# Optimization experiments

Measured on AMD Instinct MI355X. Metric: run time of the kernel, lower is better.

Reference implementation:

```python
import jax, jax.numpy as jnp
import numpy as np

B, N_ANG, LX, LY, LZ = 2, 120, 128, 128, 128


def _rotate_z(vol, phi):
    """Rotate vol [B,Lx,Ly,Lz] by phi radians (counterclockwise) in the (x,y)
    plane about the grid center, bilinear interpolation, zero padding.
    Mirrors pytomography's rotate_detector_z (bilinear grid-sample rotate)."""
    Lx, Ly = vol.shape[1], vol.shape[2]
    dt = vol.dtype
    cx = (Lx - 1) / 2.0
    cy = (Ly - 1) / 2.0
    xs = jnp.arange(Lx, dtype=dt) - cx
    ys = jnp.arange(Ly, dtype=dt) - cy
    X, Y = jnp.meshgrid(xs, ys, indexing="ij")  # [Lx,Ly]
    c, s = jnp.cos(phi), jnp.sin(phi)
    # inverse rotation maps each output pixel to its source location
    sx = c * X + s * Y + cx
    sy = -s * X + c * Y + cy
    x0 = jnp.floor(sx)
    y0 = jnp.floor(sy)
    wx = (sx - x0)[None, :, :, None]
    wy = (sy - y0)[None, :, :, None]
    x0i = x0.astype(jnp.int32)
    y0i = y0.astype(jnp.int32)

    def gather(xi, yi):
        valid = (xi >= 0) & (xi < Lx) & (yi >= 0) & (yi < Ly)
        xic = jnp.clip(xi, 0, Lx - 1)
        yic = jnp.clip(yi, 0, Ly - 1)
        v = vol[:, xic, yic, :]  # [B,Lx,Ly,Lz]
        return v * valid.astype(dt)[None, :, :, None]

    v00 = gather(x0i, y0i)
    v01 = gather(x0i, y0i + 1)
    v10 = gather(x0i + 1, y0i)
    v11 = gather(x0i + 1, y0i + 1)
    return (v00 * (1 - wx) * (1 - wy) + v01 * (1 - wx) * wy
            + v10 * wx * (1 - wy) + v11 * wx * wy)


def setup_inputs() -> dict:
    key = jax.random.key(0)
    image = jax.random.uniform(key, (B, N_ANG, LY, LZ), dtype=jnp.float32)
    angles = jnp.linspace(0.0, 360.0, N_ANG, endpoint=False).astype(jnp.float32)
    return {"image": image, "angles": angles}


def reference(image, angles, delta=1e-11):
    # image: [B, N_angles, Lr, Lz]; angles in degrees.
    Bn, Na, Lr, Lz = image.shape
    Lx = Ly = Lr
    dt = image.dtype
    phis = -jnp.deg2rad(angles).astype(dt)  # negative=True -> back-rotation

    def step(carry, inp):
        obj_acc, norm_acc = carry
        proj, phi = inp  # proj: [B, Lr, Lz]
        # image[:, i].unsqueeze(1) * ones([B, Lx, Ly, Lz]): broadcast along x
        obj_i = jnp.broadcast_to(proj[:, None, :, :], (Bn, Lx, Ly, Lz))
        norm_i = jnp.ones((Bn, Lx, Ly, Lz), dt)
        obj_acc = obj_acc + _rotate_z(obj_i, phi)
        norm_acc = norm_acc + _rotate_z(norm_i, phi)
        return (obj_acc, norm_acc), None

    init = (jnp.zeros((Bn, Lx, Ly, Lz), dt), jnp.zeros((Bn, Lx, Ly, Lz), dt))
    (obj, norm), _ = jax.lax.scan(step, init, (jnp.swapaxes(image, 0, 1), phis))
    return obj / (norm + jnp.asarray(delta, dt))
```

## Files before the change

### kernel.cpp

```cpp
#include <hip/hip_runtime.h>

namespace {

constexpr int L     = 128;
constexpr int NANG  = 120;
constexpr int NPTS  = 16;
constexpr size_t H16_BYTES = (size_t)2 * NANG * L * L * 2;

typedef __fp16 f16x2 __attribute__((ext_vector_type(2)));
typedef __fp16 f16x4 __attribute__((ext_vector_type(4)));
typedef float  f32x4 __attribute__((ext_vector_type(4)));

__global__ __launch_bounds__(256) void cvt16_kernel(const float* __restrict__ in,
                                                    unsigned* __restrict__ out) {
    const int i = ((int)blockIdx.x * 256 + (int)threadIdx.x) * 4;
    const float4 v = *reinterpret_cast<const float4*>(in + i);
    f16x2 a = __builtin_amdgcn_cvt_pkrtz(v.x, v.y);
    f16x2 b = __builtin_amdgcn_cvt_pkrtz(v.z, v.w);
    uint2 st;
    st.x = *reinterpret_cast<unsigned*>(&a);
    st.y = *reinterpret_cast<unsigned*>(&b);
    *reinterpret_cast<uint2*>(out + i / 2) = st;
}

template <bool F16>
__global__ __launch_bounds__(512, 8) void bp_kernel(
    const void* __restrict__ imgv,
    const float* __restrict__ angles,
    float* __restrict__ out)
{
    constexpr unsigned SLICE = F16 ? 32768u : 65536u;
    constexpr unsigned ROWB  = F16 ? 256u  : 512u;
    constexpr int      RSH   = F16 ? 8 : 9;

    __shared__ alignas(16) unsigned long long aftab[NANG * 2 * NPTS];
    __shared__ float2   acs[NANG];
    __shared__ unsigned arloB[NANG];
    __shared__ alignas(16) float nrmtab[NPTS];

    const int tid = threadIdx.x;
    const int bid = (int)blockIdx.x;
    const int n   = ((bid & 7) << 7) | (bid >> 3);
    int xt = 0, yt = 0;
#pragma unroll
    for (int i = 0; i < 5; ++i) {
        xt |= ((n >> (2 * i)) & 1) << i;
        yt |= ((n >> (2 * i + 1)) & 1) << i;
    }
    const int xb = xt * 4, yb = yt * 4;
    const float cx = (L - 1) * 0.5f;

    if (tid < NANG) {
        const float phi = -angles[tid] * 0.017453292519943295f;
        float s, c;
        sincosf(phi, &s, &c);
        const float X0 = (float)xb - cx,  X1 = (float)(xb + 3) - cx;
        const float Y0 = (float)yb - cx,  Y1 = (float)(yb + 3) - cx;
        const float a00 = -s * X0 + c * Y0 + cx;
        const float a01 = -s * X0 + c * Y1 + cx;
        const float a10 = -s * X1 + c * Y0 + cx;
        const float a11 = -s * X1 + c * Y1 + cx;
        const float symin = fminf(fminf(a00, a01), fminf(a10, a11));
        acs[tid]   = make_float2(c, s);
        arloB[tid] = (unsigned)min(max((int)floorf(symin) - 1, 0), 120) << RSH;
    }
    if (tid < NPTS) nrmtab[tid] = 0.f;
    __syncthreads();

    float wsum = 0.f;
#pragma unroll
    for (int k = 0; k < 4; ++k) {
        const int e = tid + k * 512;
        if (e < NANG * NPTS) {
            const int p = e & 15;
            const int a = e >> 4;
            const float2 cs = acs[a];
            const int rlo = (int)(arloB[a] >> RSH);
            const float X = (float)(xb + (p >> 2)) - cx;
            const float Y = (float)(yb + (p & 3)) - cx;
            const float sx =  cs.x * X + cs.y * Y + cx;
            const float sy = -cs.y * X + cs.x * Y + cx;
            const float x0f = floorf(sx), y0f = floorf(sy);
            const float wx = sx - x0f,    wy = sy - y0f;
            const int x0 = (int)x0f, y0 = (int)y0f;
            const float mx0 = (x0 >= 0  && x0 <  L)     ? 1.f : 0.f;
            const float mx1 = (x0 >= -1 && x0 <= L - 2) ? 1.f : 0.f;
            const float my0 = (y0 >= 0  && y0 <  L)     ? 1.f : 0.f;
            const float my1 = (y0 >= -1 && y0 <= L - 2) ? 1.f : 0.f;
            const float A   = (1.f - wx) * mx0 + wx * mx1;
            float w0f = (1.f - wy) * my0 * A;
            float w1f = wy * my1 * A;
            const int y0c = min(max(y0, 0), L - 1);
            const int y1c = min(max(y0 + 1, 0), L - 1);
            const int s0  = min(max(y0c - rlo, 0), 7);
            const int s1  = min(max(y1c - rlo, 0), 7);
            if (s0 == s1) { w0f += w1f; w1f = 0.f; }
            f16x2 wh = __builtin_amdgcn_cvt_pkrtz(w0f, w1f);
            const unsigned wbits = *reinterpret_cast<unsigned*>(&wh);
            const unsigned t  = (unsigned)s0 & 3u;
            const int      q0 = s0 >> 2;
            const unsigned long long W = (unsigned long long)wbits << (t * 16u);
            const unsigned long long spill =
                (t == 3u) ? (unsigned long long)(wbits >> 16) : 0ull;
            aftab[a * 32 + p]      = (q0 == 0) ? W : 0ull;
            aftab[a * 32 + 16 + p] = (q0 == 1) ? W : spill;
            wsum += w0f + w1f;
        }
    }
    atomicAdd(&nrmtab[tid & 15], wsum);
    __syncthreads();

    const int wave  = tid >> 6;
    const int lane  = tid & 63;
    const int quad  = lane >> 4;
    const int lhalf = lane & 15;
    const int sel   = quad >> 1;
    const int lq    = quad & 1;
    const int b     = wave & 1;
    const int zq2   = wave >> 1;
    const char* __restrict__ imgc = (const char*)imgv;

    const unsigned bbase_s = __builtin_amdgcn_readfirstlane((unsigned)(b * NANG) * SLICE);
    const unsigned voffc = (unsigned)sel * SLICE
                         + (unsigned)(lq * 4) * ROWB
                         + (unsigned)(zq2 * 32 + 2 * lhalf) * (F16 ? 2u : 4u);

    f32x4 acc[2] = {};

    auto issue = [&](unsigned* r, float2* rfp, unsigned long long& afs, int pr) {
        afs = aftab[pr * 64 + lane];
        const unsigned rlB = arloB[2 * pr + sel];
        const char* pa = imgc + (bbase_s + (unsigned)(2 * pr) * SLICE);
        const unsigned voff = voffc + rlB;
        if constexpr (F16) {
#pragma unroll
            for (int j = 0; j < 4; ++j)
                r[j] = *(const unsigned*)(pa + (voff + (unsigned)j * ROWB));
        } else {
#pragma unroll
            for (int j = 0; j < 4; ++j)
                rfp[j] = *(const float2*)(pa + (voff + (unsigned)j * ROWB));
        }
    };
    auto compute = [&](const unsigned* r, const float2* rfp, unsigned long long afu) {
        union { unsigned long long u; f16x4 v; } c; c.u = afu;
        f16x4 bf0, bf1;
        if constexpr (F16) {
            union { unsigned u[2]; f16x4 v; } b0, b1;
            b0.u[0] = __builtin_amdgcn_perm(r[1], r[0], 0x05040100u);
            b0.u[1] = __builtin_amdgcn_perm(r[3], r[2], 0x05040100u);
            b1.u[0] = __builtin_amdgcn_perm(r[1], r[0], 0x07060302u);
            b1.u[1] = __builtin_amdgcn_perm(r[3], r[2], 0x07060302u);
            bf0 = b0.v; bf1 = b1.v;
        } else {
            const f16x2 h0a = __builtin_amdgcn_cvt_pkrtz(rfp[0].x, rfp[1].x);
            const f16x2 h0b = __builtin_amdgcn_cvt_pkrtz(rfp[2].x, rfp[3].x);
            const f16x2 h1a = __builtin_amdgcn_cvt_pkrtz(rfp[0].y, rfp[1].y);
            const f16x2 h1b = __builtin_amdgcn_cvt_pkrtz(rfp[2].y, rfp[3].y);
            bf0 = f16x4{h0a.x, h0a.y, h0b.x, h0b.y};
            bf1 = f16x4{h1a.x, h1a.y, h1b.x, h1b.y};
        }
        acc[0] = __builtin_amdgcn_mfma_f32_16x16x16f16(c.v, bf0, acc[0], 0, 0, 0);
        acc[1] = __builtin_amdgcn_mfma_f32_16x16x16f16(c.v, bf1, acc[1], 0, 0, 0);
    };

    unsigned ru0[4], ru1[4], ru2[4], ru3[4];
    float2   rf0[4], rf1[4], rf2[4], rf3[4];
    unsigned long long af0, af1, af2, af3;

    issue(ru0, rf0, af0, 0);
    issue(ru1, rf1, af1, 1);
    issue(ru2, rf2, af2, 2);

    for (int p = 0; p < 60; p += 4) {
        if (p + 3 < 60) issue(ru3, rf3, af3, p + 3);
        compute(ru0, rf0, af0);
        if (p + 4 < 60) issue(ru0, rf0, af0, p + 4);
        compute(ru1, rf1, af1);
        if (p + 5 < 60) issue(ru1, rf1, af1, p + 5);
        compute(ru2, rf2, af2);
        if (p + 6 < 60) issue(ru2, rf2, af2, p + 6);
        compute(ru3, rf3, af3);
    }

    const float4 nrm4 = *(const float4*)&nrmtab[quad * 4];
    const float iv[4] = { 1.f / (nrm4.x + 1e-11f), 1.f / (nrm4.y + 1e-11f),
                          1.f / (nrm4.z + 1e-11f), 1.f / (nrm4.w + 1e-11f) };
    const int zb = zq2 * 32 + 2 * lhalf;
#pragma unroll
    for (int r = 0; r < 4; ++r) {
        const int pnt = quad * 4 + r;
        const int x = xb + (pnt >> 2);
        const int y = yb + (pnt & 3);
        const float2 o = make_float2(acc[0][r] * iv[r], acc[1][r] * iv[r]);
        *reinterpret_cast<float2*>(&out[(((size_t)(b * L + x)) * L + y) * L + zb]) = o;
    }
}

}

extern "C" void kernel_launch(void* const* d_in, const int* in_sizes, int n_in,
                              void* d_out, int out_size, void* d_ws, size_t ws_size,
                              hipStream_t stream) {
    const float* image  = (const float*)d_in[0];
    const float* angles = (const float*)d_in[1];
    float* out = (float*)d_out;
    (void)in_sizes; (void)n_in; (void)out_size;

    dim3 grid(1024);
    if (d_ws != nullptr && ws_size >= H16_BYTES) {
        cvt16_kernel<<<dim3(3840), 256, 0, stream>>>(image, (unsigned*)d_ws);
        bp_kernel<true><<<grid, 512, 0, stream>>>(d_ws, angles, out);
    } else {
        bp_kernel<false><<<grid, 512, 0, stream>>>(image, angles, out);
    }
}
```

Before: 102.0 us.

## Split angle loop across wave groups with LDS reduction and wider z loads

Each wave now covers 64 z-values with 8-byte (f16) or 16-byte (f32) loads and four MFMA accumulators instead of two, and the eight waves split into two sets that each process half the angle pairs. The partial sums from the second set are reduced through LDS, reusing the angle table buffer, before the first set normalizes and writes float4 outputs. The aim is a shorter serial dependency chain per wave and wider memory transactions. In exchange it adds more accumulator registers, two block barriers and an LDS reduction, and half the waves sit idle during the final write.

```diff
diff --git a/kernel.cpp b/kernel.cpp
--- a/kernel.cpp
+++ b/kernel.cpp
@@ -117,17 +117,20 @@
     const int sel   = quad >> 1;
     const int lq    = quad & 1;
     const int b     = wave & 1;
-    const int zq2   = wave >> 1;
+    const int zh    = (wave >> 1) & 1;
+    const int aset  = wave >> 2;
     const char* __restrict__ imgc = (const char*)imgv;
 
     const unsigned bbase_s = __builtin_amdgcn_readfirstlane((unsigned)(b * NANG) * SLICE);
     const unsigned voffc = (unsigned)sel * SLICE
                          + (unsigned)(lq * 4) * ROWB
-                         + (unsigned)(zq2 * 32 + 2 * lhalf) * (F16 ? 2u : 4u);
-
-    f32x4 acc[2] = {};
-
-    auto issue = [&](unsigned* r, float2* rfp, unsigned long long& afs, int pr) {
+                         + (unsigned)(zh * 64 + 4 * lhalf) * (F16 ? 2u : 4u);
+    const int p0 = aset * 30;
+
+    f32x4 acc[4] = {};
+
+    auto issue = [&](uint2* r, float4* rfp, unsigned long long& afs, int i) {
+        const int pr = p0 + i;
         afs = aftab[pr * 64 + lane];
         const unsigned rlB = arloB[2 * pr + sel];
         const char* pa = imgc + (bbase_s + (unsigned)(2 * pr) * SLICE);
@@ -135,65 +138,86 @@
         if constexpr (F16) {
 #pragma unroll
             for (int j = 0; j < 4; ++j)
-                r[j] = *(const unsigned*)(pa + (voff + (unsigned)j * ROWB));
+                r[j] = *(const uint2*)(pa + (voff + (unsigned)j * ROWB));
         } else {
 #pragma unroll
             for (int j = 0; j < 4; ++j)
-                rfp[j] = *(const float2*)(pa + (voff + (unsigned)j * ROWB));
+                rfp[j] = *(const float4*)(pa + (voff + (unsigned)j * ROWB));
         }
     };
-    auto compute = [&](const unsigned* r, const float2* rfp, unsigned long long afu) {
+    auto compute = [&](const uint2* r, const float4* rfp, unsigned long long afu) {
         union { unsigned long long u; f16x4 v; } c; c.u = afu;
-        f16x4 bf0, bf1;
+        f16x4 bf[4];
         if constexpr (F16) {
-            union { unsigned u[2]; f16x4 v; } b0, b1;
-            b0.u[0] = __builtin_amdgcn_perm(r[1], r[0], 0x05040100u);
-            b0.u[1] = __builtin_amdgcn_perm(r[3], r[2], 0x05040100u);
-            b1.u[0] = __builtin_amdgcn_perm(r[1], r[0], 0x07060302u);
-            b1.u[1] = __builtin_amdgcn_perm(r[3], r[2], 0x07060302u);
-            bf0 = b0.v; bf1 = b1.v;
+            union { unsigned u[2]; f16x4 v; } t;
+            t.u[0] = __builtin_amdgcn_perm(r[1].x, r[0].x, 0x05040100u);
+            t.u[1] = __builtin_amdgcn_perm(r[3].x, r[2].x, 0x05040100u);
+            bf[0] = t.v;
+            t.u[0] = __builtin_amdgcn_perm(r[1].x, r[0].x, 0x07060302u);
+            t.u[1] = __builtin_amdgcn_perm(r[3].x, r[2].x, 0x07060302u);
+            bf[1] = t.v;
+            t.u[0] = __builtin_amdgcn_perm(r[1].y, r[0].y, 0x05040100u);
+            t.u[1] = __builtin_amdgcn_perm(r[3].y, r[2].y, 0x05040100u);
+            bf[2] = t.v;
+            t.u[0] = __builtin_amdgcn_perm(r[1].y, r[0].y, 0x07060302u);
+            t.u[1] = __builtin_amdgcn_perm(r[3].y, r[2].y, 0x07060302u);
+            bf[3] = t.v;
         } else {
-            const f16x2 h0a = __builtin_amdgcn_cvt_pkrtz(rfp[0].x, rfp[1].x);
-            const f16x2 h0b = __builtin_amdgcn_cvt_pkrtz(rfp[2].x, rfp[3].x);
-            const f16x2 h1a = __builtin_amdgcn_cvt_pkrtz(rfp[0].y, rfp[1].y);
-            const f16x2 h1b = __builtin_amdgcn_cvt_pkrtz(rfp[2].y, rfp[3].y);
-            bf0 = f16x4{h0a.x, h0a.y, h0b.x, h0b.y};
-            bf1 = f16x4{h1a.x, h1a.y, h1b.x, h1b.y};
-        }
-        acc[0] = __builtin_amdgcn_mfma_f32_16x16x16f16(c.v, bf0, acc[0], 0, 0, 0);
-        acc[1] = __builtin_amdgcn_mfma_f32_16x16x16f16(c.v, bf1, acc[1], 0, 0, 0);
+#pragma unroll
+            for (int k = 0; k < 4; ++k) {
+                const f16x2 ha = __builtin_amdgcn_cvt_pkrtz(rfp[0][k], rfp[1][k]);
+                const f16x2 hb = __builtin_amdgcn_cvt_pkrtz(rfp[2][k], rfp[3][k]);
+                bf[k] = f16x4{ha.x, ha.y, hb.x, hb.y};
+            }
+        }
+#pragma unroll
+        for (int k = 0; k < 4; ++k)
+            acc[k] = __builtin_amdgcn_mfma_f32_16x16x16f16(c.v, bf[k], acc[k], 0, 0, 0);
     };
 
-    unsigned ru0[4], ru1[4], ru2[4], ru3[4];
-    float2   rf0[4], rf1[4], rf2[4], rf3[4];
-    unsigned long long af0, af1, af2, af3;
+    uint2  ru0[4], ru1[4], ru2[4];
+    float4 rf0[4], rf1[4], rf2[4];
+    unsigned long long af0, af1, af2;
 
     issue(ru0, rf0, af0, 0);
     issue(ru1, rf1, af1, 1);
-    issue(ru2, rf2, af2, 2);
-
-    for (int p = 0; p < 60; p += 4) {
-        if (p + 3 < 60) issue(ru3, rf3, af3, p + 3);
+
+    for (int i = 0; i < 30; i += 3) {
+        if (i + 2 < 30) issue(ru2, rf2, af2, i + 2);
         compute(ru0, rf0, af0);
-        if (p + 4 < 60) issue(ru0, rf0, af0, p + 4);
+        if (i + 3 < 30) issue(ru0, rf0, af0, i + 3);
         compute(ru1, rf1, af1);
-        if (p + 5 < 60) issue(ru1, rf1, af1, p + 5);
+        if (i + 4 < 30) issue(ru1, rf1, af1, i + 4);
         compute(ru2, rf2, af2);
-        if (p + 6 < 60) issue(ru2, rf2, af2, p + 6);
-        compute(ru3, rf3, af3);
-    }
-
-    const float4 nrm4 = *(const float4*)&nrmtab[quad * 4];
-    const float iv[4] = { 1.f / (nrm4.x + 1e-11f), 1.f / (nrm4.y + 1e-11f),
-                          1.f / (nrm4.z + 1e-11f), 1.f / (nrm4.w + 1e-11f) };
-    const int zb = zq2 * 32 + 2 * lhalf;
-#pragma unroll
-    for (int r = 0; r < 4; ++r) {
-        const int pnt = quad * 4 + r;
-        const int x = xb + (pnt >> 2);
-        const int y = yb + (pnt & 3);
-        const float2 o = make_float2(acc[0][r] * iv[r], acc[1][r] * iv[r]);
-        *reinterpret_cast<float2*>(&out[(((size_t)(b * L + x)) * L + y) * L + zb]) = o;
+    }
+
+    __syncthreads();
+    float4* red = reinterpret_cast<float4*>(aftab);
+    if (aset == 1) {
+#pragma unroll
+        for (int k = 0; k < 4; ++k)
+            red[k * 256 + (wave & 3) * 64 + lane] = *(const float4*)&acc[k];
+    }
+    __syncthreads();
+    if (aset == 0) {
+#pragma unroll
+        for (int k = 0; k < 4; ++k) {
+            const float4 o = red[k * 256 + (wave & 3) * 64 + lane];
+            acc[k][0] += o.x; acc[k][1] += o.y; acc[k][2] += o.z; acc[k][3] += o.w;
+        }
+        const float4 nrm4 = *(const float4*)&nrmtab[quad * 4];
+        const float iv[4] = { 1.f / (nrm4.x + 1e-11f), 1.f / (nrm4.y + 1e-11f),
+                              1.f / (nrm4.z + 1e-11f), 1.f / (nrm4.w + 1e-11f) };
+        const int zb = zh * 64 + 4 * lhalf;
+#pragma unroll
+        for (int r = 0; r < 4; ++r) {
+            const int pnt = quad * 4 + r;
+            const int x = xb + (pnt >> 2);
+            const int y = yb + (pnt & 3);
+            const float4 o = make_float4(acc[0][r] * iv[r], acc[1][r] * iv[r],
+                                         acc[2][r] * iv[r], acc[3][r] * iv[r]);
+            *reinterpret_cast<float4*>(&out[(((size_t)(b * L + x)) * L + y) * L + zb]) = o;
+        }
     }
 }
 
```

Result: slower. 104.8 us (+2.8%).
